# Kernel tuning notes

Measured on AMD Instinct MI355X. Metric: run time of the kernel, lower is better.

## Reference

```python
import jax, jax.numpy as jnp
import numpy as np

# dims (match init_kwargs)
L, D, H, K = 8, 384, 6, 64            # layers, hidden, rwkv heads, rwkv head dim
DI, MH, HD, DS, CK = 768, 12, 64, 64, 4  # mamba: d_inner, heads, head_dim, d_state, conv kernel
V, B, T = 32000, 1, 1024


def _rms(x, w, eps=1e-6):
    return w * x * jax.lax.rsqrt(jnp.mean(x * x, axis=-1, keepdims=True) + eps)


def _rwkv6(xn, Wr, Wk, Wv, Wg, Ww, w_bias, u, gn_w, gn_b, Wo):
    # RWKV6: data-dependent diagonal-decay linear attention
    Bb, Tt, Dd = xn.shape
    proj = lambda W: (xn @ W).reshape(Bb, Tt, H, K)
    r, k, v = proj(Wr), proj(Wk), proj(Wv)
    g = xn @ Wg                                        # [B,T,D]
    w = (xn @ Ww + w_bias).reshape(Bb, Tt, H, K)
    decay = jnp.exp(-jnp.exp(w))                       # in (0,1)

    def step(S, inp):                                  # S: [B,H,K,K] (key x value)
        r_t, k_t, v_t, d_t = inp                       # each [B,H,K]
        kv = k_t[..., :, None] * v_t[..., None, :]     # [B,H,K,K]
        o = jnp.einsum('bhk,bhkv->bhv', r_t, S + u[None, :, :, None] * kv)
        S = d_t[..., None] * S + kv
        return S, o

    tm = lambda a: jnp.moveaxis(a, 1, 0)               # time-major
    S0 = jnp.zeros((Bb, H, K, K), xn.dtype)
    _, o = jax.lax.scan(step, S0, (tm(r), tm(k), tm(v), tm(decay)))
    o = jnp.moveaxis(o, 0, 1)                          # [B,T,H,K]
    # per-head GroupNorm
    mu = jnp.mean(o, -1, keepdims=True)
    var = jnp.var(o, -1, keepdims=True)
    o = (o - mu) * jax.lax.rsqrt(var + 1e-5) * gn_w.reshape(H, K) + gn_b.reshape(H, K)
    o = o.reshape(Bb, Tt, Dd) * jax.nn.silu(g)
    return o @ Wo


def _mamba2(xn, W_in, conv_w, conv_b, dt_bias, A_log, Dp, mn_w, W_out):
    # Mamba2: selective scan with scalar A per head
    Bb, Tt, Dd = xn.shape
    zxbcdt = xn @ W_in                                 # [B,T, 2*DI + 2*DS + MH]
    z = zxbcdt[..., :DI]
    xBC = zxbcdt[..., DI:DI + DI + 2 * DS]
    dt = jax.nn.softplus(zxbcdt[..., -MH:] + dt_bias)  # [B,T,MH]
    # causal depthwise conv1d, kernel CK
    xp = jnp.pad(xBC, ((0, 0), (CK - 1, 0), (0, 0)))
    xBC = sum(xp[:, j:j + Tt, :] * conv_w[:, j] for j in range(CK)) + conv_b
    xBC = jax.nn.silu(xBC)
    xs = xBC[..., :DI].reshape(Bb, Tt, MH, HD)
    Bm = xBC[..., DI:DI + DS]                          # [B,T,DS]
    Cm = xBC[..., DI + DS:]                            # [B,T,DS]
    A = -jnp.exp(A_log)                                # [MH]

    def step(S, inp):                                  # S: [B,MH,HD,DS]
        x_t, B_t, C_t, dt_t = inp                      # [B,MH,HD],[B,DS],[B,DS],[B,MH]
        dA = jnp.exp(dt_t * A)                         # [B,MH]
        S = dA[..., None, None] * S + (dt_t[..., None] * x_t)[..., None] * B_t[:, None, None, :]
        y = jnp.einsum('bhps,bs->bhp', S, C_t) + Dp[None, :, None] * x_t
        return S, y

    tm = lambda a: jnp.moveaxis(a, 1, 0)
    S0 = jnp.zeros((Bb, MH, HD, DS), xn.dtype)
    _, y = jax.lax.scan(step, S0, (tm(xs), tm(Bm), tm(Cm), tm(dt)))
    y = jnp.moveaxis(y, 0, 1).reshape(Bb, Tt, DI)
    y = _rms(y * jax.nn.silu(z), mn_w)                 # gated RMSNorm
    return y @ W_out


def _forward(x, embed, ln_w, Wr, Wk, Wv, Wg, Ww, w_bias, u, gn_w, gn_b, Wo,
             W_in, conv_w, conv_b, dt_bias, A_log, Dp, mn_w, W_out,
             gw, gb, ffn_ln_w, ffn_w1, ffn_w2, ln_out_w):
    h = jnp.take(embed, x, axis=0)                     # [B,T,D]
    for i in range(L):
        xn = _rms(h, ln_w[i])
        o_r = _rwkv6(xn, Wr[i], Wk[i], Wv[i], Wg[i], Ww[i], w_bias[i], u[i], gn_w[i], gn_b[i], Wo[i])
        o_m = _mamba2(xn, W_in[i], conv_w[i], conv_b[i], dt_bias[i], A_log[i], Dp[i], mn_w[i], W_out[i])
        gate = jax.nn.sigmoid(jnp.concatenate([o_r, o_m], -1) @ gw[i] + gb[i])  # [B,T,1]
        h = h + gate * o_r + (1.0 - gate) * o_m
        hn = _rms(h, ffn_ln_w[i])
        h = h + jax.nn.gelu(hn @ ffn_w1[i], approximate=False) @ ffn_w2[i]
    h = _rms(h, ln_out_w)
    return h @ embed.T                                 # tied head -> [B,T,V]


def setup_inputs() -> dict:
    key = jax.random.key(0)
    ks = iter(jax.random.split(key, 32))
    n = lambda shape, s=0.02: jax.random.normal(next(ks), shape, jnp.float32) * s
    d = {}
    d['x'] = jax.random.randint(next(ks), (B, T), 0, V)
    d['embed'] = n((V, D))
    d['ln_w'] = jnp.ones((L, D), jnp.float32)
    d['Wr'] = n((L, D, D)); d['Wk'] = n((L, D, D)); d['Wv'] = n((L, D, D))
    d['Wg'] = n((L, D, D)); d['Ww'] = n((L, D, D))
    d['w_bias'] = n((L, D), 0.5)
    d['u'] = n((L, H, K), 0.5)
    d['gn_w'] = jnp.ones((L, D), jnp.float32)
    d['gn_b'] = jnp.zeros((L, D), jnp.float32)
    d['Wo'] = n((L, D, D))
    d['W_in'] = n((L, D, 2 * DI + 2 * DS + MH))
    d['conv_w'] = n((L, DI + 2 * DS, CK), 0.2)
    d['conv_b'] = jnp.zeros((L, DI + 2 * DS), jnp.float32)
    d['dt_bias'] = jax.random.uniform(next(ks), (L, MH), jnp.float32, -4.0, -1.0)
    d['A_log'] = jnp.log(jax.random.uniform(next(ks), (L, MH), jnp.float32, 1.0, 16.0))
    d['Dp'] = jnp.ones((L, MH), jnp.float32)
    d['mn_w'] = jnp.ones((L, DI), jnp.float32)
    d['W_out'] = n((L, DI, D))
    d['gw'] = n((L, 2 * D, 1), 0.01)
    d['gb'] = jnp.full((L, 1), float(np.log(0.3 / 0.7)), jnp.float32)
    d['ffn_ln_w'] = jnp.ones((L, D), jnp.float32)
    d['ffn_w1'] = n((L, D, 4 * D))
    d['ffn_w2'] = n((L, 4 * D, D))
    d['ln_out_w'] = jnp.ones((D,), jnp.float32)
    return d


def reference(x, embed, ln_w, Wr, Wk, Wv, Wg, Ww, w_bias, u, gn_w, gn_b, Wo,
              W_in, conv_w, conv_b, dt_bias, A_log, Dp, mn_w, W_out,
              gw, gb, ffn_ln_w, ffn_w1, ffn_w2, ln_out_w):
    return _forward(x, embed, ln_w, Wr, Wk, Wv, Wg, Ww, w_bias, u, gn_w, gn_b, Wo,
                    W_in, conv_w, conv_b, dt_bias, A_log, Dp, mn_w, W_out,
                    gw, gb, ffn_ln_w, ffn_w1, ffn_w2, ln_out_w)
```

## Files before the change

### kernel.cpp

```cpp
#include <hip/hip_runtime.h>
#include <math.h>

#define TT 1024
#define DD 384
#define NH 6
#define DI 768
#define MH 12
#define DS 64
#define NL 8
#define XDIM 1676
#define CONVC 896
#define NV 32000
#define PZS 3712
#define G_OFF 1152
#define W_OFF 1536
#define Z_OFF 1920
#define XBC_OFF 2688
#define DT_OFF 3584
#define CHK 32
#define NCH 32

typedef __attribute__((ext_vector_type(8))) short short8;
typedef __attribute__((ext_vector_type(4))) float f32x4;

__device__ __forceinline__ float siluf(float x) { return x / (1.f + expf(-x)); }
__device__ __forceinline__ float sigmoidf_(float x) { return 1.f / (1.f + expf(-x)); }
__device__ __forceinline__ float geluf(float x) {
  return 0.5f * x * (1.f + erff(x * 0.70710678118654752440f));
}
__device__ __forceinline__ unsigned short f2b(float x) {
  union { float f; unsigned int u; } v; v.f = x;
  unsigned int r = v.u + 0x7fffu + ((v.u >> 16) & 1u);
  return (unsigned short)(r >> 16);
}

#define GLDS(gp, lp) __builtin_amdgcn_global_load_lds( \
    (const __attribute__((address_space(1))) void*)(gp), \
    (__attribute__((address_space(3))) void*)(lp), 16, 0, 0)

template<int EPI>
__global__ __launch_bounds__(256) void gemm_bf16(
    const unsigned short* __restrict__ A, const unsigned short* __restrict__ Bt,
    float* __restrict__ C, unsigned short* __restrict__ Cb, int N, int K, int ldC)
{
  __shared__ unsigned short As[4096];
  __shared__ unsigned short Bs[4096];
  int tid = threadIdx.x;
  int wid = tid >> 6, lane = tid & 63;
  int m0 = blockIdx.y * 64, n0 = blockIdx.x * 64;
  int wr = wid >> 1, wc = wid & 1;
  int r0 = tid >> 3, ch = tid & 7;
  int scs = (ch ^ (r0 & 7)) * 8;
  const unsigned short* ga = A  + (size_t)(m0 + r0) * K + scs;
  const unsigned short* gb = Bt + (size_t)(n0 + r0) * K + scs;
  unsigned short* la = As + wid * 512;
  unsigned short* lb = Bs + wid * 512;
  int fr = lane & 15, fc = lane >> 4;
  f32x4 zz = {0.f, 0.f, 0.f, 0.f};
  f32x4 acc[2][2];
  acc[0][0] = zz; acc[0][1] = zz; acc[1][0] = zz; acc[1][1] = zz;

  int kper = K / (int)gridDim.z;
  int ks = blockIdx.z * kper, ke = ks + kper;
  size_t row32 = (size_t)32 * K;
  for (int k0 = ks; k0 < ke; k0 += 64) {
    GLDS(ga + k0, la);
    GLDS(ga + k0 + row32, la + 2048);
    GLDS(gb + k0, lb);
    GLDS(gb + k0 + row32, lb + 2048);
    __syncthreads();
#pragma unroll
    for (int kh = 0; kh < 2; ++kh) {
      short8 af[2], bf[2];
#pragma unroll
      for (int mg = 0; mg < 2; ++mg) {
        int ar = wr * 32 + mg * 16 + fr;
        af[mg] = *reinterpret_cast<const short8*>(&As[ar * 64 + (((kh * 4 + fc) ^ (ar & 7)) * 8)]);
      }
#pragma unroll
      for (int ng = 0; ng < 2; ++ng) {
        int br = wc * 32 + ng * 16 + fr;
        bf[ng] = *reinterpret_cast<const short8*>(&Bs[br * 64 + (((kh * 4 + fc) ^ (br & 7)) * 8)]);
      }
#pragma unroll
      for (int mg = 0; mg < 2; ++mg)
#pragma unroll
        for (int ng = 0; ng < 2; ++ng)
          acc[mg][ng] = __builtin_amdgcn_mfma_f32_16x16x32_bf16(af[mg], bf[ng], acc[mg][ng], 0, 0, 0);
    }
    __syncthreads();
  }
#pragma unroll
  for (int mg = 0; mg < 2; ++mg)
#pragma unroll
    for (int ng = 0; ng < 2; ++ng) {
      int col = n0 + wc * 32 + ng * 16 + fr;
      if (col < N) {
#pragma unroll
        for (int j = 0; j < 4; ++j) {
          int row = m0 + wr * 32 + mg * 16 + fc * 4 + j;
          if (EPI == 1)      Cb[(size_t)row * ldC + col] = f2b(geluf(acc[mg][ng][j]));
          else if (EPI == 3) atomicAdd(&C[(size_t)row * ldC + col], acc[mg][ng][j]);
          else               C[(size_t)row * ldC + col]  = acc[mg][ng][j];
        }
      }
    }
}

__global__ __launch_bounds__(256) void gemm_dual(
    const unsigned short* __restrict__ A0, const unsigned short* __restrict__ B0t,
    float* __restrict__ C0, int K0, int ld0, int nx0, int nb0,
    const unsigned short* __restrict__ A1, const unsigned short* __restrict__ B1t,
    float* __restrict__ C1, int K1, int ld1, int nx1)
{
  __shared__ unsigned short As[4096];
  __shared__ unsigned short Bs[4096];
  int b = blockIdx.x;
  const unsigned short *A, *Bt; float* C; int K, ldC, bx, by;
  if (b < nb0) { A = A0; Bt = B0t; C = C0; K = K0; ldC = ld0; bx = b % nx0; by = b / nx0; }
  else { b -= nb0; A = A1; Bt = B1t; C = C1; K = K1; ldC = ld1; bx = b % nx1; by = b / nx1; }
  int tid = threadIdx.x;
  int wid = tid >> 6, lane = tid & 63;
  int m0 = by * 64, n0 = bx * 64;
  int wr = wid >> 1, wc = wid & 1;
  int r0 = tid >> 3, ch = tid & 7;
  int scs = (ch ^ (r0 & 7)) * 8;
  const unsigned short* ga = A  + (size_t)(m0 + r0) * K + scs;
  const unsigned short* gb = Bt + (size_t)(n0 + r0) * K + scs;
  unsigned short* la = As + wid * 512;
  unsigned short* lb = Bs + wid * 512;
  int fr = lane & 15, fc = lane >> 4;
  f32x4 zz = {0.f, 0.f, 0.f, 0.f};
  f32x4 acc[2][2];
  acc[0][0] = zz; acc[0][1] = zz; acc[1][0] = zz; acc[1][1] = zz;
  size_t row32 = (size_t)32 * K;
  for (int k0 = 0; k0 < K; k0 += 64) {
    GLDS(ga + k0, la);
    GLDS(ga + k0 + row32, la + 2048);
    GLDS(gb + k0, lb);
    GLDS(gb + k0 + row32, lb + 2048);
    __syncthreads();
#pragma unroll
    for (int kh = 0; kh < 2; ++kh) {
      short8 af[2], bf[2];
#pragma unroll
      for (int mg = 0; mg < 2; ++mg) {
        int ar = wr * 32 + mg * 16 + fr;
        af[mg] = *reinterpret_cast<const short8*>(&As[ar * 64 + (((kh * 4 + fc) ^ (ar & 7)) * 8)]);
      }
#pragma unroll
      for (int ng = 0; ng < 2; ++ng) {
        int br = wc * 32 + ng * 16 + fr;
        bf[ng] = *reinterpret_cast<const short8*>(&Bs[br * 64 + (((kh * 4 + fc) ^ (br & 7)) * 8)]);
      }
#pragma unroll
      for (int mg = 0; mg < 2; ++mg)
#pragma unroll
        for (int ng = 0; ng < 2; ++ng)
          acc[mg][ng] = __builtin_amdgcn_mfma_f32_16x16x32_bf16(af[mg], bf[ng], acc[mg][ng], 0, 0, 0);
    }
    __syncthreads();
  }
#pragma unroll
  for (int mg = 0; mg < 2; ++mg)
#pragma unroll
    for (int ng = 0; ng < 2; ++ng) {
      int col = n0 + wc * 32 + ng * 16 + fr;
#pragma unroll
      for (int j = 0; j < 4; ++j) {
        int row = m0 + wr * 32 + mg * 16 + fc * 4 + j;
        C[(size_t)row * ldC + col] = acc[mg][ng][j];
      }
    }
}

__global__ __launch_bounds__(256) void gemm128(
    const unsigned short* __restrict__ A, const unsigned short* __restrict__ Bt,
    float* __restrict__ C, int N, int K, int ldC)
{
  __shared__ __align__(16) char smraw[32768];
  unsigned short* As = (unsigned short*)smraw;
  unsigned short* Bs = (unsigned short*)smraw + 8192;
  int tid = threadIdx.x;
  int wid = tid >> 6, lane = tid & 63;
  int bb = blockIdx.x;
  int xcd = bb & 7, ii = bb >> 3;
  int tt = xcd * 250 + ii;
  int m0 = (tt & 7) * 128, n0 = (tt >> 3) * 128;
  int wr = wid >> 1, wc = wid & 1;
  int r0 = tid >> 3, ch = tid & 7;
  int scs = (ch ^ (r0 & 7)) * 8;
  const unsigned short* ga = A  + (size_t)(m0 + r0) * K + scs;
  const unsigned short* gb = Bt + (size_t)(n0 + r0) * K + scs;
  int fr = lane & 15, fc = lane >> 4;
  f32x4 zz = {0.f, 0.f, 0.f, 0.f};
  f32x4 acc[4][4];
#pragma unroll
  for (int i = 0; i < 4; i++)
#pragma unroll
    for (int j = 0; j < 4; j++) acc[i][j] = zz;

  size_t row32 = (size_t)32 * K;
  for (int k0 = 0; k0 < K; k0 += 64) {
#pragma unroll
    for (int i = 0; i < 4; ++i) {
      GLDS(ga + k0 + i * row32, As + i * 2048 + wid * 512);
      GLDS(gb + k0 + i * row32, Bs + i * 2048 + wid * 512);
    }
    __syncthreads();
#pragma unroll
    for (int kh = 0; kh < 2; ++kh) {
      short8 af[4], bf[4];
#pragma unroll
      for (int mg = 0; mg < 4; ++mg) {
        int ar = wr * 64 + mg * 16 + fr;
        af[mg] = *reinterpret_cast<const short8*>(&As[ar * 64 + (((kh * 4 + fc) ^ (ar & 7)) * 8)]);
      }
#pragma unroll
      for (int ng = 0; ng < 4; ++ng) {
        int br = wc * 64 + ng * 16 + fr;
        bf[ng] = *reinterpret_cast<const short8*>(&Bs[br * 64 + (((kh * 4 + fc) ^ (br & 7)) * 8)]);
      }
#pragma unroll
      for (int mg = 0; mg < 4; ++mg)
#pragma unroll
        for (int ng = 0; ng < 4; ++ng)
          acc[mg][ng] = __builtin_amdgcn_mfma_f32_16x16x32_bf16(af[mg], bf[ng], acc[mg][ng], 0, 0, 0);
    }
    __syncthreads();
  }
  float* wst = (float*)smraw + wid * 1088;
  int rr = lane >> 2, q = (lane & 3) * 16;
#pragma unroll
  for (int mg = 0; mg < 4; ++mg) {
#pragma unroll
    for (int ng = 0; ng < 4; ++ng)
#pragma unroll
      for (int j = 0; j < 4; ++j)
        wst[(fc * 4 + j) * 68 + ng * 16 + fr] = acc[mg][ng][j];
    __syncthreads();
    int row = m0 + wr * 64 + mg * 16 + rr;
    size_t rb = (size_t)row * ldC + n0 + wc * 64 + q;
#pragma unroll
    for (int i = 0; i < 4; ++i)
      *(float4*)&C[rb + i * 4] = *(const float4*)&wst[rr * 68 + q + i * 4];
    __syncthreads();
  }
}

struct TCJob { const float* src; unsigned short* dst; int K, N, Npad, nx; size_t sStr, dStr; int tend; };
struct TC10 { TCJob j[10]; };

__global__ __launch_bounds__(256) void transconv_all(TC10 P)
{
  __shared__ float tile[32][33];
  int bid = blockIdx.x;
  int q = 0;
  while (bid >= P.j[q].tend) ++q;
  int tstart = (q == 0) ? 0 : P.j[q - 1].tend;
  TCJob jb = P.j[q];
  int local = bid - tstart;
  int bx = local % jb.nx, by = local / jb.nx;
  const float* src = jb.src + (size_t)blockIdx.y * jb.sStr;
  unsigned short* dst = jb.dst + (size_t)blockIdx.y * jb.dStr;
  int k0 = by * 32, n0 = bx * 32;
  int tx = threadIdx.x & 31, ty = threadIdx.x >> 5;
  for (int i = ty; i < 32; i += 8) {
    int k = k0 + i, n = n0 + tx;
    tile[i][tx] = (k < jb.K && n < jb.N) ? src[(size_t)k * jb.N + n] : 0.f;
  }
  __syncthreads();
  for (int i = ty; i < 32; i += 8) {
    int n = n0 + i, k = k0 + tx;
    if (n < jb.Npad && k < jb.K) dst[(size_t)n * jb.K + k] = f2b(tile[tx][i]);
  }
}

__global__ void conv_b16_kernel(const float* __restrict__ src, unsigned short* __restrict__ dst, int n)
{
  int idx = blockIdx.x * 256 + threadIdx.x;
  if (idx < n) dst[idx] = f2b(src[idx]);
}

__global__ void embed_kernel(const int* __restrict__ x, const float* __restrict__ embed,
                             float* __restrict__ h)
{
  int idx = blockIdx.x * 256 + threadIdx.x;
  if (idx < TT * DD) {
    int t = idx / DD, d = idx % DD;
    h[idx] = embed[(size_t)x[t] * DD + d];
  }
}

__global__ __launch_bounds__(256) void rms_kernel(const float* __restrict__ in,
                                                  const float* __restrict__ w,
                                                  unsigned short* __restrict__ out)
{
  int row = blockIdx.x * 4 + (threadIdx.x >> 6);
  int lane = threadIdx.x & 63;
  const float* r = in + (size_t)row * DD;
  float v[6]; float ss = 0.f;
#pragma unroll
  for (int j = 0; j < 6; ++j) { v[j] = r[lane + j * 64]; ss = fmaf(v[j], v[j], ss); }
#pragma unroll
  for (int s = 1; s < 64; s <<= 1) ss += __shfl_xor(ss, s);
  float scale = rsqrtf(ss * (1.f / DD) + 1e-6f);
#pragma unroll
  for (int j = 0; j < 6; ++j)
    out[(size_t)row * DD + lane + j * 64] = f2b(w[lane + j * 64] * v[j] * scale);
}

__global__ __launch_bounds__(256) void scanA_kernel(
    const float* __restrict__ PZ, const float* __restrict__ u, const float* __restrict__ wbias,
    float* __restrict__ so, float* __restrict__ rPb,
    float* __restrict__ MstR, float* __restrict__ DcR,
    const float* __restrict__ cw, const float* __restrict__ cbia,
    const float* __restrict__ dtbias,
    const float* __restrict__ Alog, const float* __restrict__ Dpw,
    float* __restrict__ yb, float* __restrict__ Ccb,
    float* __restrict__ MstM, float* __restrict__ DcM)
{
  __shared__ float smem[2 * 256 + 64];
  int b = blockIdx.x, tid = threadIdx.x;
  if (b < 192) {
    int h = b >> 5, c = b & 31;
    float* sbuf = smem; float* us = smem + 512;
    if (tid < 64) us[tid] = u[h * 64 + tid];
    int wv = tid >> 6, l = tid & 63;
    int vv = wv * 16 + (l & 15);
    int kc = l >> 4;
    int arr = tid >> 6, idx = tid & 63;
    int off = (arr == 0) ? 0 : (arr == 1) ? 384 : (arr == 2) ? W_OFF : 768;
    float wb = (arr == 2) ? wbias[h * 64 + idx] : 0.f;
    size_t base = (size_t)h * 64 + idx + off;
    int t0 = c * CHK;
    float S[16], Pc[16];
#pragma unroll
    for (int i = 0; i < 16; i++) { S[i] = 0.f; Pc[i] = 1.f; }
    float reg = PZ[(size_t)t0 * PZS + base];
    bool st = (wv == 0) && ((l & 15) == 0);
    for (int t = 0; t < CHK; ++t) {
      int tt = t0 + t;
      float* cb = sbuf + (t & 1) * 256;
      cb[arr * 64 + idx] = (arr == 2) ? expf(-expf(reg + wb)) : reg;
      if (t + 1 < CHK) reg = PZ[(size_t)(tt + 1) * PZS + base];
      __syncthreads();
      float vt = cb[192 + vv];
      float acc = 0.f;
      float rp[16];
#pragma unroll
      for (int i = 0; i < 16; ++i) {
        int kk = kc * 16 + i;
        float rv = cb[kk], kv = cb[64 + kk], dv = cb[128 + kk];
        rp[i] = rv * Pc[i];
        float kvv = kv * vt;
        acc = fmaf(rv, fmaf(us[kk], kvv, S[i]), acc);
        S[i] = fmaf(dv, S[i], kvv);
        Pc[i] *= dv;
      }
      acc += __shfl_xor(acc, 16);
      acc += __shfl_xor(acc, 32);
      if (l < 16) so[(size_t)tt * DD + h * 64 + vv] = acc;
      if (st) {
        float4* dst = (float4*)&rPb[(size_t)tt * DD + h * 64 + kc * 16];
        dst[0] = make_float4(rp[0], rp[1], rp[2], rp[3]);
        dst[1] = make_float4(rp[4], rp[5], rp[6], rp[7]);
        dst[2] = make_float4(rp[8], rp[9], rp[10], rp[11]);
        dst[3] = make_float4(rp[12], rp[13], rp[14], rp[15]);
      }
    }
    float* ms = MstR + (size_t)(h * NCH + c) * 4096;
    float4* msv = (float4*)&ms[vv * 64 + kc * 16];
    msv[0] = make_float4(S[0], S[1], S[2], S[3]);
    msv[1] = make_float4(S[4], S[5], S[6], S[7]);
    msv[2] = make_float4(S[8], S[9], S[10], S[11]);
    msv[3] = make_float4(S[12], S[13], S[14], S[15]);
    if (st) {
      float4* dd_ = (float4*)&DcR[(h * NCH + c) * 64 + kc * 16];
      dd_[0] = make_float4(Pc[0], Pc[1], Pc[2], Pc[3]);
      dd_[1] = make_float4(Pc[4], Pc[5], Pc[6], Pc[7]);
      dd_[2] = make_float4(Pc[8], Pc[9], Pc[10], Pc[11]);
      dd_[3] = make_float4(Pc[12], Pc[13], Pc[14], Pc[15]);
    }
  } else {
    int bb = b - 192;
    int hh = bb >> 5, c = bb & 31;
    float* sbuf = smem;
    int wv = tid >> 6, l = tid & 63;
    int p = wv * 16 + (l & 15);
    int sc = l >> 4;
    int arr = tid >> 6, idx = tid & 63;
    float A = -expf(Alog[hh]);
    float Dph = Dpw[hh];
    float dtbh = dtbias[hh];
    int t0 = c * CHK;
    float cw0 = 0.f, cw1 = 0.f, cw2 = 0.f, cw3 = 0.f, cbv = 0.f;
    float xw0 = 0.f, xw1 = 0.f, xw2 = 0.f, cur = 0.f;
    const float* xcol = nullptr;
    float reg = 0.f;
    if (arr < 3) {
      int chn = (arr == 0) ? (hh * 64 + idx) : (arr == 1) ? (DI + idx) : (DI + DS + idx);
      cw0 = cw[chn * 4 + 0]; cw1 = cw[chn * 4 + 1]; cw2 = cw[chn * 4 + 2]; cw3 = cw[chn * 4 + 3];
      cbv = cbia[chn];
      xcol = PZ + XBC_OFF + chn;
      xw0 = (t0 >= 3) ? xcol[(size_t)(t0 - 3) * PZS] : 0.f;
      xw1 = (t0 >= 2) ? xcol[(size_t)(t0 - 2) * PZS] : 0.f;
      xw2 = (t0 >= 1) ? xcol[(size_t)(t0 - 1) * PZS] : 0.f;
      cur = xcol[(size_t)t0 * PZS];
    } else {
      reg = PZ[(size_t)t0 * PZS + DT_OFF + hh];
    }
    float S[16]; float cdA = 1.f;
#pragma unroll
    for (int i = 0; i < 16; i++) S[i] = 0.f;
    bool st = (wv == 0) && ((l & 15) == 0);
    for (int t = 0; t < CHK; ++t) {
      int tt = t0 + t;
      float* cb = sbuf + (t & 1) * 256;
      if (arr < 3) {
        float cvv = fmaf(cw3, cur, fmaf(cw2, xw2, fmaf(cw1, xw1, fmaf(cw0, xw0, cbv))));
        cb[arr * 64 + idx] = siluf(cvv);
        float nx = (t + 1 < CHK) ? xcol[(size_t)(tt + 1) * PZS] : 0.f;
        xw0 = xw1; xw1 = xw2; xw2 = cur; cur = nx;
      } else {
        if (idx == 0) {
          float v = reg + dtbh;
          cb[192] = (v > 20.f) ? v : log1pf(expf(v));
        }
        if (t + 1 < CHK) reg = PZ[(size_t)(tt + 1) * PZS + DT_OFF + hh];
      }
      __syncthreads();
      float dt_ = cb[192];
      float dA = expf(dt_ * A);
      cdA *= dA;
      float xp = cb[p];
      float dtx = dt_ * xp;
      float acc = 0.f;
#pragma unroll
      for (int i = 0; i < 16; ++i) {
        int s = sc * 16 + i;
        S[i] = fmaf(dA, S[i], dtx * cb[64 + s]);
        acc = fmaf(S[i], cb[128 + s], acc);
      }
      acc += __shfl_xor(acc, 16);
      acc += __shfl_xor(acc, 32);
      if (l < 16) yb[(size_t)tt * DI + hh * 64 + p] = fmaf(Dph, xp, acc);
      if (st) {
        float4* dst = (float4*)&Ccb[(size_t)tt * DI + hh * 64 + sc * 16];
#pragma unroll
        for (int j4 = 0; j4 < 4; ++j4)
          dst[j4] = make_float4(cdA * cb[128 + sc * 16 + j4 * 4 + 0],
                                cdA * cb[128 + sc * 16 + j4 * 4 + 1],
                                cdA * cb[128 + sc * 16 + j4 * 4 + 2],
                                cdA * cb[128 + sc * 16 + j4 * 4 + 3]);
      }
    }
    float* ms = MstM + (size_t)(hh * NCH + c) * 4096;
    float4* msv = (float4*)&ms[p * 64 + sc * 16];
    msv[0] = make_float4(S[0], S[1], S[2], S[3]);
    msv[1] = make_float4(S[4], S[5], S[6], S[7]);
    msv[2] = make_float4(S[8], S[9], S[10], S[11]);
    msv[3] = make_float4(S[12], S[13], S[14], S[15]);
    if (tid == 0) DcM[hh * NCH + c] = cdA;
  }
}

__global__ __launch_bounds__(256) void corr_kernel(
    const float* __restrict__ MstR, const float* __restrict__ DcR,
    const float* __restrict__ rPb, const float* __restrict__ so,
    const float* __restrict__ MstM, const float* __restrict__ DcM,
    const float* __restrict__ Ccb, float* __restrict__ yb,
    const float* __restrict__ PZ, const float* __restrict__ gnw, const float* __restrict__ gnb,
    unsigned short* __restrict__ gob)
{
  __shared__ float S0l[64 * 68];
  __shared__ float Rl[CHK * 68];
  int b = blockIdx.x, tid = threadIdx.x;
  const float* rg; int ostride, obase, t0;
  bool rwkv = (b < 192);
  int h, cidx;
  if (rwkv) {
    h = b >> 5; cidx = b & 31;
    rg = rPb; obase = h * 64; ostride = DD;
  } else {
    int bb = b - 192; h = bb >> 5; cidx = bb & 31;
    rg = Ccb; obase = h * 64; ostride = DI;
  }
  t0 = cidx * CHK;
  float Sreg[16];
#pragma unroll
  for (int it = 0; it < 16; ++it) Sreg[it] = 0.f;
  if (rwkv) {
    int kk = tid & 63;
    for (int cp = 0; cp < cidx; ++cp) {
      float d = DcR[(h * NCH + cp) * 64 + kk];
      const float* mb = MstR + (size_t)(h * NCH + cp) * 4096;
#pragma unroll
      for (int it = 0; it < 16; ++it)
        Sreg[it] = fmaf(d, Sreg[it], mb[tid + 256 * it]);
    }
  } else {
    for (int cp = 0; cp < cidx; ++cp) {
      float d = DcM[h * NCH + cp];
      const float* mb = MstM + (size_t)(h * NCH + cp) * 4096;
#pragma unroll
      for (int it = 0; it < 16; ++it)
        Sreg[it] = fmaf(d, Sreg[it], mb[tid + 256 * it]);
    }
  }
#pragma unroll
  for (int it = 0; it < 16; ++it) {
    int gi = tid + 256 * it;
    S0l[(gi & 63) * 68 + (gi >> 6)] = Sreg[it];
  }
  {
    int t = tid >> 3, q = (tid & 7) * 8;
    const float4* src = (const float4*)&rg[(size_t)(t0 + t) * ostride + obase + q];
    float4* dst = (float4*)&Rl[t * 68 + q];
    dst[0] = src[0]; dst[1] = src[1];
  }
  __syncthreads();
  int t = tid >> 3, q = (tid & 7) * 8;
  float acc[8];
#pragma unroll
  for (int j = 0; j < 8; j++) acc[j] = 0.f;
  for (int k = 0; k < 64; ++k) {
    float rv = Rl[t * 68 + k];
    const float4* sp = (const float4*)&S0l[k * 68 + q];
    float4 s0 = sp[0], s1 = sp[1];
    acc[0] = fmaf(rv, s0.x, acc[0]);
    acc[1] = fmaf(rv, s0.y, acc[1]);
    acc[2] = fmaf(rv, s0.z, acc[2]);
    acc[3] = fmaf(rv, s0.w, acc[3]);
    acc[4] = fmaf(rv, s1.x, acc[4]);
    acc[5] = fmaf(rv, s1.y, acc[5]);
    acc[6] = fmaf(rv, s1.z, acc[6]);
    acc[7] = fmaf(rv, s1.w, acc[7]);
  }
  if (!rwkv) {
    float4* op = (float4*)&yb[(size_t)(t0 + t) * DI + obase + q];
    float4 c0 = op[0], c1 = op[1];
    c0.x += acc[0]; c0.y += acc[1]; c0.z += acc[2]; c0.w += acc[3];
    c1.x += acc[4]; c1.y += acc[5]; c1.z += acc[6]; c1.w += acc[7];
    op[0] = c0; op[1] = c1;
  } else {
    float ov[8];
    const float4* sp = (const float4*)&so[(size_t)(t0 + t) * DD + obase + q];
    float4 s0 = sp[0], s1 = sp[1];
    ov[0] = s0.x + acc[0]; ov[1] = s0.y + acc[1]; ov[2] = s0.z + acc[2]; ov[3] = s0.w + acc[3];
    ov[4] = s1.x + acc[4]; ov[5] = s1.y + acc[5]; ov[6] = s1.z + acc[6]; ov[7] = s1.w + acc[7];
    float m_ = 0.f;
#pragma unroll
    for (int j = 0; j < 8; j++) m_ += ov[j];
    m_ += __shfl_xor(m_, 1); m_ += __shfl_xor(m_, 2); m_ += __shfl_xor(m_, 4);
    float mu = m_ * (1.f / 64.f);
    float vv = 0.f;
#pragma unroll
    for (int j = 0; j < 8; j++) { float d = ov[j] - mu; vv = fmaf(d, d, vv); }
    vv += __shfl_xor(vv, 1); vv += __shfl_xor(vv, 2); vv += __shfl_xor(vv, 4);
    float rstd = rsqrtf(vv * (1.f / 64.f) + 1e-5f);
#pragma unroll
    for (int j = 0; j < 8; j++) {
      int d = obase + q + j;
      float gv = PZ[(size_t)(t0 + t) * PZS + G_OFF + d];
      float o = fmaf((ov[j] - mu) * rstd, gnw[d], gnb[d]) * siluf(gv);
      gob[(size_t)(t0 + t) * DD + d] = f2b(o);
    }
  }
}

__global__ __launch_bounds__(256) void mamba_norm_kernel(const float* __restrict__ yb,
    const float* __restrict__ PZ, const float* __restrict__ mnw, unsigned short* __restrict__ out)
{
  int row = blockIdx.x * 4 + (threadIdx.x >> 6);
  int lane = threadIdx.x & 63;
  float v[12]; float ss = 0.f;
#pragma unroll
  for (int j = 0; j < 12; ++j) {
    int c = lane + j * 64;
    float z = PZ[(size_t)row * PZS + Z_OFF + c];
    float t = yb[(size_t)row * DI + c] * siluf(z);
    v[j] = t; ss = fmaf(t, t, ss);
  }
#pragma unroll
  for (int s = 1; s < 64; s <<= 1) ss += __shfl_xor(ss, s);
  float scale = rsqrtf(ss * (1.f / DI) + 1e-6f);
#pragma unroll
  for (int j = 0; j < 12; ++j) {
    int c = lane + j * 64;
    out[(size_t)row * DI + c] = f2b(v[j] * scale * mnw[c]);
  }
}

__global__ __launch_bounds__(256) void gate_rms_kernel(const float* __restrict__ orb,
    const float* __restrict__ omb, const float* __restrict__ gw,
    const float* __restrict__ gb, const float* __restrict__ flnw,
    float* __restrict__ h, unsigned short* __restrict__ xnb)
{
  int row = blockIdx.x * 4 + (threadIdx.x >> 6);
  int lane = threadIdx.x & 63;
  float a[6], bq[6]; float ss = 0.f;
#pragma unroll
  for (int j = 0; j < 6; ++j) {
    int c = lane + j * 64;
    a[j] = orb[(size_t)row * DD + c]; bq[j] = omb[(size_t)row * DD + c];
    ss += a[j] * gw[c] + bq[j] * gw[DD + c];
  }
#pragma unroll
  for (int s = 1; s < 64; s <<= 1) ss += __shfl_xor(ss, s);
  float gate = sigmoidf_(ss + gb[0]);
  float hn[6]; float ss2 = 0.f;
#pragma unroll
  for (int j = 0; j < 6; ++j) {
    int c = lane + j * 64;
    size_t ix = (size_t)row * DD + c;
    hn[j] = h[ix] + gate * a[j] + (1.f - gate) * bq[j];
    h[ix] = hn[j];
    ss2 = fmaf(hn[j], hn[j], ss2);
  }
#pragma unroll
  for (int s = 1; s < 64; s <<= 1) ss2 += __shfl_xor(ss2, s);
  float scale = rsqrtf(ss2 * (1.f / DD) + 1e-6f);
#pragma unroll
  for (int j = 0; j < 6; ++j) {
    int c = lane + j * 64;
    xnb[(size_t)row * DD + c] = f2b(flnw[c] * hn[j] * scale);
  }
}

extern "C" void kernel_launch(void* const* d_in, const int* in_sizes, int n_in,
                              void* d_out, int out_size, void* d_ws, size_t ws_size,
                              hipStream_t stream)
{
  const int*   x        = (const int*)  d_in[0];
  const float* embed    = (const float*)d_in[1];
  const float* ln_w     = (const float*)d_in[2];
  const float* Wr       = (const float*)d_in[3];
  const float* Wk       = (const float*)d_in[4];
  const float* Wv       = (const float*)d_in[5];
  const float* Wg       = (const float*)d_in[6];
  const float* Ww       = (const float*)d_in[7];
  const float* w_bias   = (const float*)d_in[8];
  const float* u        = (const float*)d_in[9];
  const float* gn_w     = (const float*)d_in[10];
  const float* gn_b     = (const float*)d_in[11];
  const float* Wo       = (const float*)d_in[12];
  const float* W_in     = (const float*)d_in[13];
  const float* conv_w   = (const float*)d_in[14];
  const float* conv_b   = (const float*)d_in[15];
  const float* dt_bias  = (const float*)d_in[16];
  const float* A_log    = (const float*)d_in[17];
  const float* Dp       = (const float*)d_in[18];
  const float* mn_w     = (const float*)d_in[19];
  const float* W_out    = (const float*)d_in[20];
  const float* gw       = (const float*)d_in[21];
  const float* gb       = (const float*)d_in[22];
  const float* ffn_ln_w = (const float*)d_in[23];
  const float* ffn_w1   = (const float*)d_in[24];
  const float* ffn_w2   = (const float*)d_in[25];
  const float* ln_out_w = (const float*)d_in[26];

  char* base = (char*)d_ws;
  size_t off = 0;
  auto alloc = [&](size_t bytes) { off = (off + 255) & ~(size_t)255; void* p = base + off; off += bytes; return p; };

  float* h    = (float*)alloc((size_t)TT * DD * 4);
  float* PZ   = (float*)alloc((size_t)TT * PZS * 4);
  float* yb   = (float*)alloc((size_t)TT * DI * 4);
  float* so   = (float*)alloc((size_t)TT * DD * 4);
  float* orb  = (float*)alloc((size_t)TT * DD * 4);
  float* omb  = (float*)alloc((size_t)TT * DD * 4);
  float* rPb  = (float*)alloc((size_t)TT * DD * 4);
  float* Ccb  = (float*)alloc((size_t)TT * DI * 4);
  float* MstR = (float*)alloc((size_t)NH * NCH * 4096 * 4);
  float* DcR  = (float*)alloc((size_t)NH * NCH * 64 * 4);
  float* MstM = (float*)alloc((size_t)MH * NCH * 4096 * 4);
  float* DcM  = (float*)alloc((size_t)MH * NCH * 4);
  unsigned short* xnb = (unsigned short*)alloc((size_t)TT * DD * 2);
  unsigned short* gob = (unsigned short*)alloc((size_t)TT * DD * 2);
  unsigned short* ynb = (unsigned short*)alloc((size_t)TT * DI * 2);
  unsigned short* fhb = (unsigned short*)alloc((size_t)TT * 1536 * 2);
  unsigned short* WallT = (unsigned short*)alloc((size_t)NL * PZS * 384 * 2);
  unsigned short* WoT   = (unsigned short*)alloc((size_t)NL * 384 * 384 * 2);
  unsigned short* WoutT = (unsigned short*)alloc((size_t)NL * 384 * 768 * 2);
  unsigned short* F1T   = (unsigned short*)alloc((size_t)NL * 1536 * 384 * 2);
  unsigned short* F2T   = (unsigned short*)alloc((size_t)NL * 384 * 1536 * 2);
  unsigned short* embB  = (unsigned short*)alloc((size_t)NV * DD * 2);
  (void)ws_size; (void)in_sizes; (void)n_in; (void)out_size;

  dim3 blk(256);
  int gTD = (TT * DD + 255) / 256;

  TC10 tc;
  int te = 0;
  auto setjob = [&](int q, const float* src, unsigned short* dst, int K, int N, int Npad,
                    int nx, int ny, size_t sStr, size_t dStr) {
    te += nx * ny;
    tc.j[q] = TCJob{src, dst, K, N, Npad, nx, sStr, dStr, te};
  };
  setjob(0, Wr, WallT + (size_t)0 * 384 * 384, 384, 384, 384, 12, 12, (size_t)384 * 384, (size_t)PZS * 384);
  setjob(1, Wk, WallT + (size_t)1 * 384 * 384, 384, 384, 384, 12, 12, (size_t)384 * 384, (size_t)PZS * 384);
  setjob(2, Wv, WallT + (size_t)2 * 384 * 384, 384, 384, 384, 12, 12, (size_t)384 * 384, (size_t)PZS * 384);
  setjob(3, Wg, WallT + (size_t)3 * 384 * 384, 384, 384, 384, 12, 12, (size_t)384 * 384, (size_t)PZS * 384);
  setjob(4, Ww, WallT + (size_t)4 * 384 * 384, 384, 384, 384, 12, 12, (size_t)384 * 384, (size_t)PZS * 384);
  setjob(5, W_in, WallT + (size_t)1920 * 384, 384, XDIM, 1792, 56, 12, (size_t)384 * XDIM, (size_t)PZS * 384);
  setjob(6, Wo, WoT, 384, 384, 384, 12, 12, (size_t)384 * 384, (size_t)384 * 384);
  setjob(7, W_out, WoutT, 768, 384, 384, 12, 24, (size_t)768 * 384, (size_t)384 * 768);
  setjob(8, ffn_w1, F1T, 384, 1536, 1536, 48, 12, (size_t)384 * 1536, (size_t)1536 * 384);
  setjob(9, ffn_w2, F2T, 1536, 384, 384, 12, 48, (size_t)1536 * 384, (size_t)384 * 1536);
  transconv_all<<<dim3(te, 8), blk, 0, stream>>>(tc);
  conv_b16_kernel<<<(NV * DD + 255) / 256, blk, 0, stream>>>(embed, embB, NV * DD);
  embed_kernel<<<gTD, blk, 0, stream>>>(x, embed, h);

  for (int i = 0; i < NL; ++i) {
    rms_kernel<<<256, blk, 0, stream>>>(h, ln_w + (size_t)i * DD, xnb);

    gemm_bf16<0><<<dim3(58, 16), blk, 0, stream>>>(
        xnb, WallT + (size_t)i * PZS * 384, PZ, nullptr, PZS, 384, PZS);

    scanA_kernel<<<576, blk, 0, stream>>>(PZ, u + (size_t)i * NH * 64, w_bias + (size_t)i * DD,
                                          so, rPb, MstR, DcR,
                                          conv_w + (size_t)i * CONVC * 4, conv_b + (size_t)i * CONVC,
                                          dt_bias + (size_t)i * MH,
                                          A_log + (size_t)i * MH, Dp + (size_t)i * MH,
                                          yb, Ccb, MstM, DcM);
    corr_kernel<<<576, blk, 0, stream>>>(MstR, DcR, rPb, so, MstM, DcM, Ccb, yb,
                                         PZ, gn_w + (size_t)i * DD, gn_b + (size_t)i * DD, gob);

    mamba_norm_kernel<<<256, blk, 0, stream>>>(yb, PZ, mn_w + (size_t)i * DI, ynb);

    gemm_dual<<<192, blk, 0, stream>>>(
        gob, WoT + (size_t)i * 384 * 384, orb, 384, DD, 6, 96,
        ynb, WoutT + (size_t)i * 384 * 768, omb, 768, DD, 6);

    gate_rms_kernel<<<256, blk, 0, stream>>>(orb, omb, gw + (size_t)i * 2 * DD, gb + i,
                                             ffn_ln_w + (size_t)i * DD, h, xnb);

    gemm_bf16<1><<<dim3(24, 16), blk, 0, stream>>>(
        xnb, F1T + (size_t)i * 1536 * 384, nullptr, fhb, 1536, 384, 1536);
    gemm_bf16<3><<<dim3(6, 16, 4), blk, 0, stream>>>(
        fhb, F2T + (size_t)i * 384 * 1536, h, nullptr, 384, 1536, 384);
  }

  rms_kernel<<<256, blk, 0, stream>>>(h, ln_out_w, xnb);
  gemm128<<<dim3(2000), blk, 0, stream>>>(
      xnb, embB, (float*)d_out, NV, 384, NV);
}
```

Before: 993.0 us.

## Double-buffer LDS tiles in GEMM kernels to overlap loads with MFMA

Each of the three bf16 GEMM kernels now keeps two LDS buffers per operand. It prefetches the first K-tile before the loop and, in each iteration, issues the async global-to-LDS loads for the next tile before running the MFMAs on the current one. This drops one barrier per iteration and is meant to hide global-load latency behind matrix math. In exchange, LDS use per block doubles (64 KB for the 128x128 kernel), which may lower occupancy.

```diff
diff --git a/kernel.cpp b/kernel.cpp
--- a/kernel.cpp
+++ b/kernel.cpp
@@ -43,8 +43,8 @@
     const unsigned short* __restrict__ A, const unsigned short* __restrict__ Bt,
     float* __restrict__ C, unsigned short* __restrict__ Cb, int N, int K, int ldC)
 {
-  __shared__ unsigned short As[4096];
-  __shared__ unsigned short Bs[4096];
+  __shared__ unsigned short As[8192];
+  __shared__ unsigned short Bs[8192];
   int tid = threadIdx.x;
   int wid = tid >> 6, lane = tid & 63;
   int m0 = blockIdx.y * 64, n0 = blockIdx.x * 64;
@@ -53,8 +53,6 @@
   int scs = (ch ^ (r0 & 7)) * 8;
   const unsigned short* ga = A  + (size_t)(m0 + r0) * K + scs;
   const unsigned short* gb = Bt + (size_t)(n0 + r0) * K + scs;
-  unsigned short* la = As + wid * 512;
-  unsigned short* lb = Bs + wid * 512;
   int fr = lane & 15, fc = lane >> 4;
   f32x4 zz = {0.f, 0.f, 0.f, 0.f};
   f32x4 acc[2][2];
@@ -63,24 +61,34 @@
   int kper = K / (int)gridDim.z;
   int ks = blockIdx.z * kper, ke = ks + kper;
   size_t row32 = (size_t)32 * K;
+  GLDS(ga + ks, As + wid * 512);
+  GLDS(ga + ks + row32, As + 2048 + wid * 512);
+  GLDS(gb + ks, Bs + wid * 512);
+  GLDS(gb + ks + row32, Bs + 2048 + wid * 512);
+  __syncthreads();
+  int cur = 0;
   for (int k0 = ks; k0 < ke; k0 += 64) {
-    GLDS(ga + k0, la);
-    GLDS(ga + k0 + row32, la + 2048);
-    GLDS(gb + k0, lb);
-    GLDS(gb + k0 + row32, lb + 2048);
-    __syncthreads();
+    int nk = k0 + 64;
+    if (nk < ke) {
+      int nb = (cur ^ 1) * 4096;
+      GLDS(ga + nk, As + nb + wid * 512);
+      GLDS(ga + nk + row32, As + nb + 2048 + wid * 512);
+      GLDS(gb + nk, Bs + nb + wid * 512);
+      GLDS(gb + nk + row32, Bs + nb + 2048 + wid * 512);
+    }
+    int cb = cur * 4096;
 #pragma unroll
     for (int kh = 0; kh < 2; ++kh) {
       short8 af[2], bf[2];
 #pragma unroll
       for (int mg = 0; mg < 2; ++mg) {
         int ar = wr * 32 + mg * 16 + fr;
-        af[mg] = *reinterpret_cast<const short8*>(&As[ar * 64 + (((kh * 4 + fc) ^ (ar & 7)) * 8)]);
+        af[mg] = *reinterpret_cast<const short8*>(&As[cb + ar * 64 + (((kh * 4 + fc) ^ (ar & 7)) * 8)]);
       }
 #pragma unroll
       for (int ng = 0; ng < 2; ++ng) {
         int br = wc * 32 + ng * 16 + fr;
-        bf[ng] = *reinterpret_cast<const short8*>(&Bs[br * 64 + (((kh * 4 + fc) ^ (br & 7)) * 8)]);
+        bf[ng] = *reinterpret_cast<const short8*>(&Bs[cb + br * 64 + (((kh * 4 + fc) ^ (br & 7)) * 8)]);
       }
 #pragma unroll
       for (int mg = 0; mg < 2; ++mg)
@@ -89,6 +97,7 @@
           acc[mg][ng] = __builtin_amdgcn_mfma_f32_16x16x32_bf16(af[mg], bf[ng], acc[mg][ng], 0, 0, 0);
     }
     __syncthreads();
+    cur ^= 1;
   }
 #pragma unroll
   for (int mg = 0; mg < 2; ++mg)
@@ -113,8 +122,8 @@
     const unsigned short* __restrict__ A1, const unsigned short* __restrict__ B1t,
     float* __restrict__ C1, int K1, int ld1, int nx1)
 {
-  __shared__ unsigned short As[4096];
-  __shared__ unsigned short Bs[4096];
+  __shared__ unsigned short As[8192];
+  __shared__ unsigned short Bs[8192];
   int b = blockIdx.x;
   const unsigned short *A, *Bt; float* C; int K, ldC, bx, by;
   if (b < nb0) { A = A0; Bt = B0t; C = C0; K = K0; ldC = ld0; bx = b % nx0; by = b / nx0; }
@@ -127,31 +136,39 @@
   int scs = (ch ^ (r0 & 7)) * 8;
   const unsigned short* ga = A  + (size_t)(m0 + r0) * K + scs;
   const unsigned short* gb = Bt + (size_t)(n0 + r0) * K + scs;
-  unsigned short* la = As + wid * 512;
-  unsigned short* lb = Bs + wid * 512;
   int fr = lane & 15, fc = lane >> 4;
   f32x4 zz = {0.f, 0.f, 0.f, 0.f};
   f32x4 acc[2][2];
   acc[0][0] = zz; acc[0][1] = zz; acc[1][0] = zz; acc[1][1] = zz;
   size_t row32 = (size_t)32 * K;
+  GLDS(ga, As + wid * 512);
+  GLDS(ga + row32, As + 2048 + wid * 512);
+  GLDS(gb, Bs + wid * 512);
+  GLDS(gb + row32, Bs + 2048 + wid * 512);
+  __syncthreads();
+  int cur = 0;
   for (int k0 = 0; k0 < K; k0 += 64) {
-    GLDS(ga + k0, la);
-    GLDS(ga + k0 + row32, la + 2048);
-    GLDS(gb + k0, lb);
-    GLDS(gb + k0 + row32, lb + 2048);
-    __syncthreads();
+    int nk = k0 + 64;
+    if (nk < K) {
+      int nb = (cur ^ 1) * 4096;
+      GLDS(ga + nk, As + nb + wid * 512);
+      GLDS(ga + nk + row32, As + nb + 2048 + wid * 512);
+      GLDS(gb + nk, Bs + nb + wid * 512);
+      GLDS(gb + nk + row32, Bs + nb + 2048 + wid * 512);
+    }
+    int cb = cur * 4096;
 #pragma unroll
     for (int kh = 0; kh < 2; ++kh) {
       short8 af[2], bf[2];
 #pragma unroll
       for (int mg = 0; mg < 2; ++mg) {
         int ar = wr * 32 + mg * 16 + fr;
-        af[mg] = *reinterpret_cast<const short8*>(&As[ar * 64 + (((kh * 4 + fc) ^ (ar & 7)) * 8)]);
+        af[mg] = *reinterpret_cast<const short8*>(&As[cb + ar * 64 + (((kh * 4 + fc) ^ (ar & 7)) * 8)]);
       }
 #pragma unroll
       for (int ng = 0; ng < 2; ++ng) {
         int br = wc * 32 + ng * 16 + fr;
-        bf[ng] = *reinterpret_cast<const short8*>(&Bs[br * 64 + (((kh * 4 + fc) ^ (br & 7)) * 8)]);
+        bf[ng] = *reinterpret_cast<const short8*>(&Bs[cb + br * 64 + (((kh * 4 + fc) ^ (br & 7)) * 8)]);
       }
 #pragma unroll
       for (int mg = 0; mg < 2; ++mg)
@@ -160,6 +177,7 @@
           acc[mg][ng] = __builtin_amdgcn_mfma_f32_16x16x32_bf16(af[mg], bf[ng], acc[mg][ng], 0, 0, 0);
     }
     __syncthreads();
+    cur ^= 1;
   }
 #pragma unroll
   for (int mg = 0; mg < 2; ++mg)
@@ -178,9 +196,9 @@
     const unsigned short* __restrict__ A, const unsigned short* __restrict__ Bt,
     float* __restrict__ C, int N, int K, int ldC)
 {
-  __shared__ __align__(16) char smraw[32768];
+  __shared__ __align__(16) char smraw[65536];
   unsigned short* As = (unsigned short*)smraw;
-  unsigned short* Bs = (unsigned short*)smraw + 8192;
+  unsigned short* Bs = (unsigned short*)smraw + 16384;
   int tid = threadIdx.x;
   int wid = tid >> 6, lane = tid & 63;
   int bb = blockIdx.x;
@@ -201,25 +219,36 @@
     for (int j = 0; j < 4; j++) acc[i][j] = zz;
 
   size_t row32 = (size_t)32 * K;
+#pragma unroll
+  for (int i = 0; i < 4; ++i) {
+    GLDS(ga + i * row32, As + i * 2048 + wid * 512);
+    GLDS(gb + i * row32, Bs + i * 2048 + wid * 512);
+  }
+  __syncthreads();
+  int cur = 0;
   for (int k0 = 0; k0 < K; k0 += 64) {
-#pragma unroll
-    for (int i = 0; i < 4; ++i) {
-      GLDS(ga + k0 + i * row32, As + i * 2048 + wid * 512);
-      GLDS(gb + k0 + i * row32, Bs + i * 2048 + wid * 512);
-    }
-    __syncthreads();
+    int nk = k0 + 64;
+    if (nk < K) {
+      int nb = (cur ^ 1) * 8192;
+#pragma unroll
+      for (int i = 0; i < 4; ++i) {
+        GLDS(ga + nk + i * row32, As + nb + i * 2048 + wid * 512);
+        GLDS(gb + nk + i * row32, Bs + nb + i * 2048 + wid * 512);
+      }
+    }
+    int cb = cur * 8192;
 #pragma unroll
     for (int kh = 0; kh < 2; ++kh) {
       short8 af[4], bf[4];
 #pragma unroll
       for (int mg = 0; mg < 4; ++mg) {
         int ar = wr * 64 + mg * 16 + fr;
-        af[mg] = *reinterpret_cast<const short8*>(&As[ar * 64 + (((kh * 4 + fc) ^ (ar & 7)) * 8)]);
+        af[mg] = *reinterpret_cast<const short8*>(&As[cb + ar * 64 + (((kh * 4 + fc) ^ (ar & 7)) * 8)]);
       }
 #pragma unroll
       for (int ng = 0; ng < 4; ++ng) {
         int br = wc * 64 + ng * 16 + fr;
-        bf[ng] = *reinterpret_cast<const short8*>(&Bs[br * 64 + (((kh * 4 + fc) ^ (br & 7)) * 8)]);
+        bf[ng] = *reinterpret_cast<const short8*>(&Bs[cb + br * 64 + (((kh * 4 + fc) ^ (br & 7)) * 8)]);
       }
 #pragma unroll
       for (int mg = 0; mg < 4; ++mg)
@@ -228,6 +257,7 @@
           acc[mg][ng] = __builtin_amdgcn_mfma_f32_16x16x32_bf16(af[mg], bf[ng], acc[mg][ng], 0, 0, 0);
     }
     __syncthreads();
+    cur ^= 1;
   }
   float* wst = (float*)smraw + wid * 1088;
   int rr = lane >> 2, q = (lane & 3) * 16;
```

After: 1.009 ms. Within noise of the previous version (+1.6%).
